# Optimization experiments

Measured on AMD Instinct MI355X. Metric: run time of the kernel, lower is better.

Reference implementation:

```python
import jax, jax.numpy as jnp
import numpy as np

N, D, H, E = 16384, 1024, 4096, 8

def setup_inputs() -> dict:
    key = jax.random.key(0)
    ks = jax.random.split(key, 7)
    s = 0.02
    return {
        "x": jax.random.normal(ks[0], (N, D), dtype=jnp.float32),
        "Ws": jax.random.normal(ks[1], (H, D), dtype=jnp.float32) * s,
        "bs": jax.random.normal(ks[2], (H,), dtype=jnp.float32) * s,
        "We": jax.random.normal(ks[3], (E, H, D), dtype=jnp.float32) * s,
        "be": jax.random.normal(ks[4], (E, H), dtype=jnp.float32) * s,
        "Wr": jax.random.normal(ks[5], (E, D), dtype=jnp.float32) * s,
        "br": jax.random.normal(ks[6], (E,), dtype=jnp.float32) * s,
    }

def reference(x, Ws, bs, We, be, Wr, br):
    # shared FFN: [N, H]
    shared = x @ Ws.T + bs
    # router: softmax over experts, top-1 via argmax (argmax(softmax)==argmax(logits), kept faithful)
    expert_scores = jax.nn.softmax(x @ Wr.T + br, axis=-1)  # [N, E]
    token_expert = jnp.argmax(expert_scores, axis=-1)       # [N]
    # mask-accumulate over the small fixed expert set (dense per-expert FFN as in source)
    routed = jnp.zeros_like(shared)
    num_experts = We.shape[0]
    for i in range(num_experts):
        mask = (token_expert == i).astype(shared.dtype)[:, None]  # [N, 1]
        routed = routed + mask * (x @ We[i].T + be[i])
    return shared + routed
```

## Files before the change

### kernel.cpp

```cpp
#include <hip/hip_runtime.h>
#include <stdint.h>

#define N_TOK 16384
#define DDIM  1024
#define HDIM  4096
#define NEXP  8
#define BM    256
#define GX    16
#define MAXMT 72
#define NWG   (GX * MAXMT)
#define KT    16
#define HT_TOTAL (KT * 4)

typedef __attribute__((ext_vector_type(8))) short short8;
typedef __attribute__((ext_vector_type(4))) float f32x4;

__device__ __forceinline__ unsigned short f2b(float f) {
    union { float f; unsigned int u; } x; x.f = f;
    unsigned int r = x.u + 0x7FFFu + ((x.u >> 16) & 1u);
    return (unsigned short)(r >> 16);
}

__global__ __launch_bounds__(256)
void k_router_cast(const float* __restrict__ x, const float* __restrict__ Wr,
                   const float* __restrict__ br, unsigned short* __restrict__ xb,
                   int* __restrict__ eid)
{
    __shared__ float wr[NEXP * DDIM];
    const int t = threadIdx.x;
    for (int i = t; i < NEXP * DDIM / 4; i += 256)
        ((float4*)wr)[i] = ((const float4*)Wr)[i];
    __syncthreads();
    const int lane = t & 63;
    const int n = blockIdx.x * 4 + (t >> 6);
    const float* xr = x + (size_t)n * DDIM;
    double acc[NEXP];
#pragma unroll
    for (int e = 0; e < NEXP; ++e) acc[e] = 0.0;
#pragma unroll
    for (int j = 0; j < 4; ++j) {
        const int d = j * 256 + lane * 4;
        float4 v = *(const float4*)(xr + d);
        unsigned long long pk =
            (unsigned long long)(f2b(v.x) | ((unsigned int)f2b(v.y) << 16)) |
            ((unsigned long long)(f2b(v.z) | ((unsigned int)f2b(v.w) << 16)) << 32);
        *(unsigned long long*)(xb + (size_t)n * DDIM + d) = pk;
#pragma unroll
        for (int e = 0; e < NEXP; ++e) {
            const float* w = wr + e * DDIM + d;
            acc[e] += (double)v.x * (double)w[0];
            acc[e] += (double)v.y * (double)w[1];
            acc[e] += (double)v.z * (double)w[2];
            acc[e] += (double)v.w * (double)w[3];
        }
    }
#pragma unroll
    for (int e = 0; e < NEXP; ++e)
#pragma unroll
        for (int off = 32; off > 0; off >>= 1)
            acc[e] += __shfl_down(acc[e], off);
    if (lane == 0) {
        double best = acc[0] + (double)br[0];
        int bi = 0;
#pragma unroll
        for (int e = 1; e < NEXP; ++e) {
            double v = acc[e] + (double)br[e];
            if (v > best) { best = v; bi = e; }
        }
        eid[n] = bi;
    }
}

__global__ __launch_bounds__(256)
void k_hist(const int* __restrict__ eid, int* __restrict__ counts)
{
    __shared__ int h[NEXP];
    const int t = threadIdx.x;
    if (t < NEXP) h[t] = 0;
    __syncthreads();
    atomicAdd(&h[eid[blockIdx.x * 256 + t]], 1);
    __syncthreads();
    if (t < NEXP && h[t]) atomicAdd(&counts[t * 16], h[t]);
}

__global__ void k_scan(const int* __restrict__ counts, int* __restrict__ texp,
                       int* __restrict__ pbase)
{
    if (threadIdx.x == 0) {
        int tt = 0;
        for (int e = 0; e < NEXP; ++e) {
            pbase[e] = tt * BM;
            const int nt = (counts[e * 16] + BM - 1) / BM;
            for (int i = 0; i < nt; ++i) texp[tt++] = e;
        }
        for (; tt < MAXMT; ++tt) texp[tt] = -1;
    }
}

__global__ __launch_bounds__(256)
void k_scatter(const int* __restrict__ eid, const int* __restrict__ pbase,
               int* __restrict__ cursors, int* __restrict__ perm)
{
    __shared__ int h[NEXP];
    __shared__ int base[NEXP];
    const int t = threadIdx.x;
    if (t < NEXP) h[t] = 0;
    __syncthreads();
    const int n = blockIdx.x * 256 + t;
    const int e = eid[n];
    const int rank = atomicAdd(&h[e], 1);
    __syncthreads();
    if (t < NEXP) base[t] = h[t] ? atomicAdd(&cursors[t * 16], h[t]) : 0;
    __syncthreads();
    perm[pbase[e] + base[e] + rank] = n;
}

__global__ __launch_bounds__(256)
void k_combine_w(const float* __restrict__ Ws, const float* __restrict__ We,
                 unsigned short* __restrict__ wc)
{
    const size_t i = ((size_t)blockIdx.x * 256 + threadIdx.x) * 8;
    const size_t hd = i & (size_t)(HDIM * DDIM - 1);
    float4 a0 = *(const float4*)(We + i);
    float4 a1 = *(const float4*)(We + i + 4);
    float4 b0 = *(const float4*)(Ws + hd);
    float4 b1 = *(const float4*)(Ws + hd + 4);
    uint4 o;
    o.x = f2b(a0.x + b0.x) | ((unsigned)f2b(a0.y + b0.y) << 16);
    o.y = f2b(a0.z + b0.z) | ((unsigned)f2b(a0.w + b0.w) << 16);
    o.z = f2b(a1.x + b1.x) | ((unsigned)f2b(a1.y + b1.y) << 16);
    o.w = f2b(a1.z + b1.z) | ((unsigned)f2b(a1.w + b1.w) << 16);
    *(uint4*)(wc + i) = o;
}

__global__ __launch_bounds__(256)
void k_combine_b(const float* __restrict__ bs, const float* __restrict__ be,
                 float* __restrict__ bc)
{
    const int i = blockIdx.x * 256 + threadIdx.x;
    bc[i] = bs[i & (HDIM - 1)] + be[i];
}

#define SBAR()   __builtin_amdgcn_s_barrier()
#define SCHED0() __builtin_amdgcn_sched_barrier(0)
#define LGKM0()  asm volatile("s_waitcnt lgkmcnt(0)" ::: "memory")

__global__ __launch_bounds__(512, 2)
void k_gemm(const unsigned short* __restrict__ X, const unsigned short* __restrict__ W,
            const float* __restrict__ bc, const int* __restrict__ perm,
            const int* __restrict__ texp, float* __restrict__ out)
{
    __shared__ unsigned short lds[65536];

    const int flat = blockIdx.x;
    const int wg = (flat & 7) * (NWG >> 3) + (flat >> 3);
    const int tm = wg / GX, tn = wg % GX;
    const int e = texp[tm];
    if (e < 0) return;

    const int t    = threadIdx.x;
    const int lane = t & 63;
    const int wid  = t >> 6;
    const int wm   = wid >> 2;
    const int wn   = wid & 3;

    const int srow   = t >> 3;
    const int schunk = (t & 7) ^ (srow & 7);
    const unsigned short* Wb0 =
        W + ((size_t)e * HDIM + (size_t)tn * 256 + srow) * DDIM + schunk * 8;
    const unsigned short* Asrc[2][2];
#pragma unroll
    for (int h = 0; h < 2; ++h)
#pragma unroll
        for (int j = 0; j < 2; ++j) {
            int tok = perm[tm * BM + h * 128 + j * 64 + srow];
            if (tok < 0) tok = 0;
            Asrc[h][j] = X + (size_t)tok * DDIM + schunk * 8;
        }
    unsigned short* dstT = lds + (t << 3);

    const int rA   = lane & 15;
    const int colk = (lane >> 4) << 3;
    const int c0   = colk ^ ((lane & 7) << 3);
    const int c1   = c0 ^ 32;
    const int aBase = ((2 + wm) << 13) + (rA << 6);
    const int bBase = ((wn >> 1) << 13) + ((wn & 1) << 12) + (rA << 6);

    f32x4 acc[8][4];
#pragma unroll
    for (int m = 0; m < 8; ++m)
#pragma unroll
        for (int n = 0; n < 4; ++n) acc[m][n] = (f32x4){0.f, 0.f, 0.f, 0.f};
    short8 fa[8][2], fb[4][2];

    auto STAGE = [&](int sigma) {
        if (sigma >= HT_TOTAL) return;
        const int st = sigma >> 2;
        const int h  = sigma & 3;
        const int kb = st << 6;
        unsigned short* d = dstT + ((st & 1) << 15) + (h << 13);
        const unsigned short *s0, *s1;
        if (h < 2) {
            const unsigned short* b = Wb0 + ((size_t)h << 17) + kb;
            s0 = b; s1 = b + (size_t)64 * DDIM;
        } else {
            s0 = Asrc[h - 2][0] + kb;
            s1 = Asrc[h - 2][1] + kb;
        }
        __builtin_amdgcn_global_load_lds(
            (const __attribute__((address_space(1))) void*)s0,
            (__attribute__((address_space(3))) void*)d, 16, 0, 0);
        __builtin_amdgcn_global_load_lds(
            (const __attribute__((address_space(1))) void*)s1,
            (__attribute__((address_space(3))) void*)(d + 4096), 16, 0, 0);
    };

#define LDA(m) \
    fa[m][0] = *(const short8*)&lds[bufOff + aBase + (m)*1024 + c0]; \
    fa[m][1] = *(const short8*)&lds[bufOff + aBase + (m)*1024 + c1];
#define LDB(n) \
    fb[n][0] = *(const short8*)&lds[bufOff + bBase + (n)*1024 + c0]; \
    fb[n][1] = *(const short8*)&lds[bufOff + bBase + (n)*1024 + c1];
#define MM(m,n) \
    acc[m][n] = __builtin_amdgcn_mfma_f32_16x16x32_bf16(fa[m][0], fb[n][0], acc[m][n], 0,0,0); \
    acc[m][n] = __builtin_amdgcn_mfma_f32_16x16x32_bf16(fa[m][1], fb[n][1], acc[m][n], 0,0,0);

#pragma unroll
    for (int s = 0; s < 7; ++s) STAGE(s);
    asm volatile("s_waitcnt vmcnt(6)" ::: "memory");
    SCHED0(); SBAR(); SCHED0();

#pragma unroll 1
    for (int tt = 0; tt < KT; ++tt) {
        const int bufOff = (tt & 1) << 15;
        const int sig = 7 + (tt << 2);
        LDB(0) LDB(1) LDA(0) LDA(1)
        STAGE(sig);
        SCHED0(); SBAR(); LGKM0(); SCHED0();
        __builtin_amdgcn_s_setprio(1);
        if (tt) { MM(6,2) MM(6,3) MM(7,2) MM(7,3) }
        MM(0,0) MM(0,1) MM(1,0) MM(1,1)
        __builtin_amdgcn_s_setprio(0);
        SCHED0(); SBAR(); SCHED0();
        LDB(2) LDB(3) LDA(2) LDA(3)
        STAGE(sig + 1);
        SCHED0(); SBAR(); LGKM0(); SCHED0();
        __builtin_amdgcn_s_setprio(1);
        MM(0,2) MM(0,3) MM(1,2) MM(1,3) MM(2,0) MM(2,1) MM(3,0) MM(3,1)
        __builtin_amdgcn_s_setprio(0);
        SCHED0(); SBAR(); SCHED0();
        LDA(4) LDA(5) LDA(6) LDA(7)
        STAGE(sig + 2);
        SCHED0(); SBAR(); LGKM0(); SCHED0();
        __builtin_amdgcn_s_setprio(1);
        MM(2,2) MM(2,3) MM(3,2) MM(3,3) MM(4,0) MM(4,1) MM(5,0) MM(5,1)
        __builtin_amdgcn_s_setprio(0);
        SCHED0(); SBAR(); SCHED0();
        STAGE(sig + 3);
        SCHED0(); SBAR(); SCHED0();
        __builtin_amdgcn_s_setprio(1);
        MM(4,2) MM(4,3) MM(5,2) MM(5,3) MM(6,0) MM(6,1) MM(7,0) MM(7,1)
        __builtin_amdgcn_s_setprio(0);
        SCHED0();
        if (tt < KT - 2)       { asm volatile("s_waitcnt vmcnt(6)" ::: "memory"); }
        else if (tt == KT - 2) { asm volatile("s_waitcnt vmcnt(0)" ::: "memory"); }
        SBAR(); SCHED0();
    }
    MM(6,2) MM(6,3) MM(7,2) MM(7,3)

    const int colBase = tn * 256 + wn * 64 + (lane & 15);
    float bias[4];
#pragma unroll
    for (int n = 0; n < 4; ++n) bias[n] = bc[e * HDIM + colBase + n * 16];
    const int rsub = (lane >> 4) * 4;
#pragma unroll
    for (int m = 0; m < 8; ++m) {
        const int rbase = tm * BM + wm * 128 + m * 16 + rsub;
        int tk[4];
#pragma unroll
        for (int j = 0; j < 4; ++j) tk[j] = perm[rbase + j];
#pragma unroll
        for (int n = 0; n < 4; ++n) {
            const int col = colBase + n * 16;
#pragma unroll
            for (int j = 0; j < 4; ++j)
                if (tk[j] >= 0) out[(size_t)tk[j] * HDIM + col] = acc[m][n][j] + bias[n];
        }
    }
#undef LDA
#undef LDB
#undef MM
}

extern "C" void kernel_launch(void* const* d_in, const int* in_sizes, int n_in,
                              void* d_out, int out_size, void* d_ws, size_t ws_size,
                              hipStream_t stream)
{
    const float* x  = (const float*)d_in[0];
    const float* Ws = (const float*)d_in[1];
    const float* bs = (const float*)d_in[2];
    const float* We = (const float*)d_in[3];
    const float* be = (const float*)d_in[4];
    const float* Wr = (const float*)d_in[5];
    const float* br = (const float*)d_in[6];
    float* out = (float*)d_out;
    char* ws = (char*)d_ws;

    unsigned short* xb  = (unsigned short*)(ws + 0);
    unsigned short* wc  = (unsigned short*)(ws + 33554432);
    float*          bc  = (float*)(ws + 100663296);
    int*            eid = (int*)(ws + 100794368);
    int*            perm= (int*)(ws + 100859904);
    int*            cnt = (int*)(ws + 100933632);
    int*            cur = (int*)(ws + 100934144);
    int*            pb  = (int*)(ws + 100934656);
    int*            texp= (int*)(ws + 100934688);

    hipMemsetAsync(perm, 0xFF, MAXMT * BM * sizeof(int), stream);
    hipMemsetAsync(cnt, 0, 1024, stream);

    k_router_cast<<<N_TOK / 4, 256, 0, stream>>>(x, Wr, br, xb, eid);
    k_combine_w<<<(NEXP * (size_t)HDIM * DDIM / 8) / 256, 256, 0, stream>>>(Ws, We, wc);
    k_combine_b<<<NEXP * HDIM / 256, 256, 0, stream>>>(bs, be, bc);
    k_hist<<<N_TOK / 256, 256, 0, stream>>>(eid, cnt);
    k_scan<<<1, 64, 0, stream>>>(cnt, texp, pb);
    k_scatter<<<N_TOK / 256, 256, 0, stream>>>(eid, pb, cur, perm);
    k_gemm<<<NWG, 512, 0, stream>>>(xb, wc, bc, perm, texp, out);
}
```

Baseline: 303.9 us.

## Make GEMM persistent over row tiles with cross-tile prefetch and bias-initialized accumulators

The grouped GEMM now launches a fixed grid of 256 persistent workgroups. Each one walks up to five M-tiles that share an N-column, keeping the global-to-LDS pipeline running across tile boundaries so there is no prologue or drain between tiles. Token indices and biases are staged in LDS up front, and accumulators start at the bias so the epilogue becomes a plain scatter store. This removes the early-exit launches for empty tiles and the per-tile pipeline fill cost, in exchange for more complex control flow and a single wave of workgroups, which may balance load unevenly.

```diff
diff --git a/kernel.cpp b/kernel.cpp
--- a/kernel.cpp
+++ b/kernel.cpp
@@ -6,11 +6,8 @@
 #define HDIM  4096
 #define NEXP  8
 #define BM    256
-#define GX    16
 #define MAXMT 72
-#define NWG   (GX * MAXMT)
-#define KT    16
-#define HT_TOTAL (KT * 4)
+#define MAXNR 5
 
 typedef __attribute__((ext_vector_type(8))) short short8;
 typedef __attribute__((ext_vector_type(4))) float f32x4;
@@ -93,6 +90,7 @@
             const int nt = (counts[e * 16] + BM - 1) / BM;
             for (int i = 0; i < nt; ++i) texp[tt++] = e;
         }
+        pbase[8] = tt;
         for (; tt < MAXMT; ++tt) texp[tt] = -1;
     }
 }
@@ -148,15 +146,19 @@
 __global__ __launch_bounds__(512, 2)
 void k_gemm(const unsigned short* __restrict__ X, const unsigned short* __restrict__ W,
             const float* __restrict__ bc, const int* __restrict__ perm,
-            const int* __restrict__ texp, float* __restrict__ out)
+            const int* __restrict__ texp, const int* __restrict__ realM_p,
+            float* __restrict__ out)
 {
     __shared__ unsigned short lds[65536];
-
-    const int flat = blockIdx.x;
-    const int wg = (flat & 7) * (NWG >> 3) + (flat >> 3);
-    const int tm = wg / GX, tn = wg % GX;
-    const int e = texp[tm];
-    if (e < 0) return;
+    __shared__ int   toksLDS[MAXNR][256];
+    __shared__ float biasLDS[MAXNR][256];
+
+    const int realM = realM_p[8];
+    const int base  = blockIdx.x;
+    const int tnr   = base & 15;
+    const int tmB   = base >> 4;
+    const int nR    = (realM - tmB + 15) >> 4;
+    const int T     = nR << 4;
 
     const int t    = threadIdx.x;
     const int lane = t & 63;
@@ -164,48 +166,77 @@
     const int wm   = wid >> 2;
     const int wn   = wid & 3;
 
-    const int srow   = t >> 3;
-    const int schunk = (t & 7) ^ (srow & 7);
-    const unsigned short* Wb0 =
-        W + ((size_t)e * HDIM + (size_t)tn * 256 + srow) * DDIM + schunk * 8;
-    const unsigned short* Asrc[2][2];
-#pragma unroll
-    for (int h = 0; h < 2; ++h)
-#pragma unroll
-        for (int j = 0; j < 2; ++j) {
-            int tok = perm[tm * BM + h * 128 + j * 64 + srow];
-            if (tok < 0) tok = 0;
-            Asrc[h][j] = X + (size_t)tok * DDIM + schunk * 8;
-        }
+    const int srow    = t >> 3;
+    const int schunkE = (((t & 7) ^ (srow & 7)) << 3);
     unsigned short* dstT = lds + (t << 3);
 
     const int rA   = lane & 15;
-    const int colk = (lane >> 4) << 3;
-    const int c0   = colk ^ ((lane & 7) << 3);
+    const int c0   = ((lane >> 4) << 3) ^ ((lane & 7) << 3);
     const int c1   = c0 ^ 32;
     const int aBase = ((2 + wm) << 13) + (rA << 6);
     const int bBase = ((wn >> 1) << 13) + ((wn & 1) << 12) + (rA << 6);
+    const int colBase = tnr * 256 + wn * 64 + rA;
+
+    int ePk = 0;
+#pragma unroll
+    for (int w = 0; w < MAXNR; ++w) {
+        const int ev = (w < nR) ? texp[tmB + (w << 4)] : 0;
+        ePk |= (ev & 15) << (w << 2);
+    }
+    if (t < 256) {
+#pragma unroll
+        for (int w = 0; w < MAXNR; ++w) {
+            if (w < nR) {
+                toksLDS[w][t] = perm[(tmB + (w << 4)) * 256 + t];
+                const int ev = (ePk >> (w << 2)) & 15;
+                biasLDS[w][t] = bc[ev * HDIM + tnr * 256 + t];
+            }
+        }
+    }
+    __syncthreads();
+
+    int tokCur[4], tokNext[4];
+#pragma unroll
+    for (int i = 0; i < 4; ++i) {
+        int a = toksLDS[0][i * 64 + srow];
+        tokCur[i] = a < 0 ? 0 : a;
+        int b = (nR > 1) ? toksLDS[1][i * 64 + srow] : 0;
+        tokNext[i] = b < 0 ? 0 : b;
+    }
 
     f32x4 acc[8][4];
-#pragma unroll
-    for (int m = 0; m < 8; ++m)
-#pragma unroll
-        for (int n = 0; n < 4; ++n) acc[m][n] = (f32x4){0.f, 0.f, 0.f, 0.f};
+    {
+        float bn[4];
+#pragma unroll
+        for (int n = 0; n < 4; ++n) bn[n] = biasLDS[0][wn * 64 + n * 16 + rA];
+#pragma unroll
+        for (int m = 0; m < 8; ++m)
+#pragma unroll
+            for (int n = 0; n < 4; ++n)
+                acc[m][n] = (f32x4){bn[n], bn[n], bn[n], bn[n]};
+    }
     short8 fa[8][2], fb[4][2];
 
-    auto STAGE = [&](int sigma) {
-        if (sigma >= HT_TOTAL) return;
-        const int st = sigma >> 2;
-        const int h  = sigma & 3;
-        const int kb = st << 6;
-        unsigned short* d = dstT + ((st & 1) << 15) + (h << 13);
+    auto STAGE = [&](int sg, int tau) {
+        if (sg >= (nR << 6)) return;
+        const int tloc = sg >> 2;
+        const int h    = sg & 3;
+        const int kb   = (tloc & 15) << 6;
+        unsigned short* d = dstT + ((tloc & 1) << 15) + (h << 13);
         const unsigned short *s0, *s1;
         if (h < 2) {
-            const unsigned short* b = Wb0 + ((size_t)h << 17) + kb;
-            s0 = b; s1 = b + (size_t)64 * DDIM;
+            const int wS = tloc >> 4;
+            const int ee = (ePk >> (wS << 2)) & 15;
+            const size_t r0 = (size_t)(ee * HDIM + tnr * 256 + h * 128 + srow) * DDIM
+                              + schunkE + kb;
+            s0 = W + r0; s1 = W + r0 + (size_t)64 * DDIM;
         } else {
-            s0 = Asrc[h - 2][0] + kb;
-            s1 = Asrc[h - 2][1] + kb;
+            const bool nxt = (tloc >> 4) != (tau >> 4);
+            const int i0 = (h - 2) << 1;
+            const int ta = nxt ? tokNext[i0]     : tokCur[i0];
+            const int tb = nxt ? tokNext[i0 + 1] : tokCur[i0 + 1];
+            s0 = X + (size_t)ta * DDIM + schunkE + kb;
+            s1 = X + (size_t)tb * DDIM + schunkE + kb;
         }
         __builtin_amdgcn_global_load_lds(
             (const __attribute__((address_space(1))) void*)s0,
@@ -226,65 +257,86 @@
     acc[m][n] = __builtin_amdgcn_mfma_f32_16x16x32_bf16(fa[m][1], fb[n][1], acc[m][n], 0,0,0);
 
 #pragma unroll
-    for (int s = 0; s < 7; ++s) STAGE(s);
+    for (int s = 0; s < 7; ++s) STAGE(s, 0);
     asm volatile("s_waitcnt vmcnt(6)" ::: "memory");
     SCHED0(); SBAR(); SCHED0();
 
+    int w = 0;
 #pragma unroll 1
-    for (int tt = 0; tt < KT; ++tt) {
-        const int bufOff = (tt & 1) << 15;
-        const int sig = 7 + (tt << 2);
+    for (int tau = 0; tau < T; ++tau) {
+        const int tt = tau & 15;
+        const int bufOff = (tau & 1) << 15;
+        const int sig = (tau << 2) + 7;
+
         LDB(0) LDB(1) LDA(0) LDA(1)
-        STAGE(sig);
+        STAGE(sig, tau);
         SCHED0(); SBAR(); LGKM0(); SCHED0();
         __builtin_amdgcn_s_setprio(1);
-        if (tt) { MM(6,2) MM(6,3) MM(7,2) MM(7,3) }
+        if (tt != 0) { MM(6,2) MM(6,3) MM(7,2) MM(7,3) }
         MM(0,0) MM(0,1) MM(1,0) MM(1,1)
         __builtin_amdgcn_s_setprio(0);
         SCHED0(); SBAR(); SCHED0();
         LDB(2) LDB(3) LDA(2) LDA(3)
-        STAGE(sig + 1);
+        STAGE(sig + 1, tau);
         SCHED0(); SBAR(); LGKM0(); SCHED0();
         __builtin_amdgcn_s_setprio(1);
         MM(0,2) MM(0,3) MM(1,2) MM(1,3) MM(2,0) MM(2,1) MM(3,0) MM(3,1)
         __builtin_amdgcn_s_setprio(0);
         SCHED0(); SBAR(); SCHED0();
         LDA(4) LDA(5) LDA(6) LDA(7)
-        STAGE(sig + 2);
+        STAGE(sig + 2, tau);
         SCHED0(); SBAR(); LGKM0(); SCHED0();
         __builtin_amdgcn_s_setprio(1);
         MM(2,2) MM(2,3) MM(3,2) MM(3,3) MM(4,0) MM(4,1) MM(5,0) MM(5,1)
         __builtin_amdgcn_s_setprio(0);
         SCHED0(); SBAR(); SCHED0();
-        STAGE(sig + 3);
+        STAGE(sig + 3, tau);
         SCHED0(); SBAR(); SCHED0();
         __builtin_amdgcn_s_setprio(1);
         MM(4,2) MM(4,3) MM(5,2) MM(5,3) MM(6,0) MM(6,1) MM(7,0) MM(7,1)
+        if (tt == 15) { MM(6,2) MM(6,3) MM(7,2) MM(7,3) }
         __builtin_amdgcn_s_setprio(0);
         SCHED0();
-        if (tt < KT - 2)       { asm volatile("s_waitcnt vmcnt(6)" ::: "memory"); }
-        else if (tt == KT - 2) { asm volatile("s_waitcnt vmcnt(0)" ::: "memory"); }
+        if (tau < T - 2)       { asm volatile("s_waitcnt vmcnt(6)" ::: "memory"); }
+        else if (tau == T - 2) { asm volatile("s_waitcnt vmcnt(0)" ::: "memory"); }
         SBAR(); SCHED0();
-    }
-    MM(6,2) MM(6,3) MM(7,2) MM(7,3)
-
-    const int colBase = tn * 256 + wn * 64 + (lane & 15);
-    float bias[4];
-#pragma unroll
-    for (int n = 0; n < 4; ++n) bias[n] = bc[e * HDIM + colBase + n * 16];
-    const int rsub = (lane >> 4) * 4;
-#pragma unroll
-    for (int m = 0; m < 8; ++m) {
-        const int rbase = tm * BM + wm * 128 + m * 16 + rsub;
-        int tk[4];
-#pragma unroll
-        for (int j = 0; j < 4; ++j) tk[j] = perm[rbase + j];
-#pragma unroll
-        for (int n = 0; n < 4; ++n) {
-            const int col = colBase + n * 16;
-#pragma unroll
-            for (int j = 0; j < 4; ++j)
-                if (tk[j] >= 0) out[(size_t)tk[j] * HDIM + col] = acc[m][n][j] + bias[n];
+
+        if (tt == 15) {
+            const int rsub = (lane >> 4) * 4;
+#pragma unroll
+            for (int m = 0; m < 8; ++m) {
+                const int rl = wm * 128 + m * 16 + rsub;
+                int tk[4];
+#pragma unroll
+                for (int j = 0; j < 4; ++j) tk[j] = toksLDS[w][rl + j];
+#pragma unroll
+                for (int n = 0; n < 4; ++n) {
+                    const int col = colBase + n * 16;
+#pragma unroll
+                    for (int j = 0; j < 4; ++j)
+                        if (tk[j] >= 0) out[(size_t)tk[j] * HDIM + col] = acc[m][n][j];
+                }
+            }
+            if (w + 1 < nR) {
+                float bn[4];
+#pragma unroll
+                for (int n = 0; n < 4; ++n) bn[n] = biasLDS[w + 1][wn * 64 + n * 16 + rA];
+#pragma unroll
+                for (int m = 0; m < 8; ++m)
+#pragma unroll
+                    for (int n = 0; n < 4; ++n)
+                        acc[m][n] = (f32x4){bn[n], bn[n], bn[n], bn[n]};
+#pragma unroll
+                for (int i = 0; i < 4; ++i) tokCur[i] = tokNext[i];
+                if (w + 2 < nR) {
+#pragma unroll
+                    for (int i = 0; i < 4; ++i) {
+                        int v = toksLDS[w + 2][i * 64 + srow];
+                        tokNext[i] = v < 0 ? 0 : v;
+                    }
+                }
+            }
+            ++w;
         }
     }
 #undef LDA
@@ -314,7 +366,7 @@
     int*            cnt = (int*)(ws + 100933632);
     int*            cur = (int*)(ws + 100934144);
     int*            pb  = (int*)(ws + 100934656);
-    int*            texp= (int*)(ws + 100934688);
+    int*            texp= (int*)(ws + 100934720);
 
     hipMemsetAsync(perm, 0xFF, MAXMT * BM * sizeof(int), stream);
     hipMemsetAsync(cnt, 0, 1024, stream);
@@ -325,5 +377,5 @@
     k_hist<<<N_TOK / 256, 256, 0, stream>>>(eid, cnt);
     k_scan<<<1, 64, 0, stream>>>(cnt, texp, pb);
     k_scatter<<<N_TOK / 256, 256, 0, stream>>>(eid, pb, cur, perm);
-    k_gemm<<<NWG, 512, 0, stream>>>(xb, wc, bc, perm, texp, out);
-}
+    k_gemm<<<256, 512, 0, stream>>>(xb, wc, bc, perm, texp, pb, out);
+}
```

Result: faster. 292.4 us (-3.8%).
